# Kernel tuning notes

Measured on AMD Instinct MI355X. Metric: run time of the kernel, lower is better.

Reference implementation:

```python
import jax, jax.numpy as jnp
import numpy as np

D_MODEL = 1024
NUM_HEADS = 16
DEPTH = D_MODEL // NUM_HEADS


def setup_inputs() -> dict:
    key = jax.random.key(0)
    ks = jax.random.split(key, 9)
    B, S = 2, 2048
    s = 1.0 / np.sqrt(D_MODEL)
    return {
        "x": jax.random.normal(ks[0], (B, S, D_MODEL), dtype=jnp.float32),
        "wq": jax.random.normal(ks[1], (D_MODEL, D_MODEL), dtype=jnp.float32) * s,
        "bq": jnp.zeros((D_MODEL,), dtype=jnp.float32),
        "wk": jax.random.normal(ks[2], (D_MODEL, D_MODEL), dtype=jnp.float32) * s,
        "bk": jnp.zeros((D_MODEL,), dtype=jnp.float32),
        "wv": jax.random.normal(ks[3], (D_MODEL, D_MODEL), dtype=jnp.float32) * s,
        "bv": jnp.zeros((D_MODEL,), dtype=jnp.float32),
        "wo": jax.random.normal(ks[4], (D_MODEL, D_MODEL), dtype=jnp.float32) * s,
        "bo": jnp.zeros((D_MODEL,), dtype=jnp.float32),
    }


def _split_heads(t):
    # [B, S, D] -> [B, H, S, depth]
    B, S, _ = t.shape
    return t.reshape(B, S, NUM_HEADS, DEPTH).transpose(0, 2, 1, 3)


def reference(x, wq, bq, wk, bk, wv, bv, wo, bo):
    B, S, _ = x.shape
    q = _split_heads(x @ wq + bq)
    k = _split_heads(x @ wk + bk)
    v = _split_heads(x @ wv + bv)
    scale = 1.0 / jnp.sqrt(jnp.asarray(DEPTH, dtype=x.dtype))
    logits = jnp.einsum("bhsd,bhtd->bhst", q, k) * scale  # [B,H,S,S]
    attn = jax.nn.softmax(logits, axis=-1)
    ctx = jnp.einsum("bhst,bhtd->bhsd", attn, v)  # [B,H,S,depth]
    concat = ctx.transpose(0, 2, 1, 3).reshape(B, S, D_MODEL)
    return concat @ wo + bo
```

## Files before the change

### kernel.cpp

```cpp
#include <hip/hip_runtime.h>
#include <hip/hip_bf16.h>

typedef __bf16 bf16;
typedef __bf16 bf16x4 __attribute__((ext_vector_type(4)));
typedef __bf16 bf16x8 __attribute__((ext_vector_type(8)));
typedef float f32x4 __attribute__((ext_vector_type(4)));

typedef __attribute__((address_space(3))) void lds_void;
typedef const __attribute__((address_space(1))) void gbl_void;

#define D_MODEL 1024
#define NHEAD 16
#define DEPTH 64
#define SEQ 2048
#define BATCH 2
#define NTOK (BATCH * SEQ)

#define Q_SCALE 0.18033688f

__global__ __launch_bounds__(256) void prep(const float* __restrict__ w0,
                                            const float* __restrict__ w1,
                                            const float* __restrict__ w2,
                                            const float* __restrict__ w3,
                                            const float* __restrict__ x,
                                            bf16* __restrict__ wtb,
                                            bf16* __restrict__ xb) {
    int z = blockIdx.z;
    int tx = threadIdx.x, ty = threadIdx.y;
    if (z < 4) {
        const float* w = (z == 0) ? w0 : (z == 1) ? w1 : (z == 2) ? w2 : w3;
        bf16* d = wtb + (size_t)z * D_MODEL * D_MODEL;
        __shared__ float tile[32][33];
        int c0 = blockIdx.x * 32;
        int r0 = blockIdx.y * 32;
#pragma unroll
        for (int i = 0; i < 4; i++)
            tile[ty + i * 8][tx] = w[(size_t)(r0 + ty + i * 8) * D_MODEL + c0 + tx];
        __syncthreads();
#pragma unroll
        for (int i = 0; i < 4; i++)
            d[(size_t)(c0 + ty + i * 8) * D_MODEL + r0 + tx] = (bf16)tile[tx][ty + i * 8];
    } else {
        int t = ty * 32 + tx;
        size_t i = ((size_t)(z - 4) * 1024 + blockIdx.y * 32 + blockIdx.x) * 256 + t;
        float4 v = ((const float4*)x)[i];
        bf16x4 o = {(bf16)v.x, (bf16)v.y, (bf16)v.z, (bf16)v.w};
        *(bf16x4*)&xb[i * 4] = o;
    }
}

__global__ __launch_bounds__(512, 2) void qkv_gemm(const bf16* __restrict__ xb,
                                                   const bf16* __restrict__ wtb,
                                                   const float* __restrict__ bq,
                                                   const float* __restrict__ bk,
                                                   const float* __restrict__ bv,
                                                   bf16* __restrict__ q,
                                                   bf16* __restrict__ k,
                                                   bf16* __restrict__ v) {
    __shared__ bf16 sm[65536];

    const int flat = blockIdx.x;
    const int wg = (flat & 7) * 24 + (flat >> 3);
    const int mt = wg & 15, nt = wg >> 4;
    const int row0 = mt << 8;
    const int z = nt >> 2;
    const int nb = (nt & 3) << 8;

    const int tid = threadIdx.x;
    const int lane = tid & 63, wave = tid >> 6;
    const int wm = wave >> 2, wn = wave & 3;
    const int quad = lane >> 4, l16 = lane & 15;
    const int kch = ((quad ^ ((l16 >> 1) & 3)) << 3);

    const int srow = lane >> 2;
    const int scg = (lane & 3) ^ ((lane >> 3) & 3);
    const int stDst = wave * 1024 + lane * 8;

    const bf16* Ag = xb + (size_t)(row0 + wave * 32 + srow) * D_MODEL + scg * 8;
    const bf16* Bg = wtb + (size_t)z * D_MODEL * D_MODEL
                   + (size_t)(nb + wave * 32 + srow) * D_MODEL + scg * 8;

    f32x4 acc[8][4] = {};
    bf16x8 bfr[4];

#define GLL(SRC, DST) __builtin_amdgcn_global_load_lds((gbl_void*)(SRC), (lds_void*)(DST), 16, 0, 0)
#define STG_A(T_, KQ_, BUF_) { \
    const bf16* s_ = Ag + (T_) * 64 + (KQ_) * 32; \
    bf16* d_ = sm + (BUF_) * 16384 + (KQ_) * 8192 + stDst; \
    GLL(s_, d_); GLL(s_ + 16 * D_MODEL, d_ + 512); }
#define STG_B(T_, KQ_, BUF_) { \
    const bf16* s_ = Bg + (T_) * 64 + (KQ_) * 32; \
    bf16* d_ = sm + 32768 + (BUF_) * 16384 + (KQ_) * 8192 + stDst; \
    GLL(s_, d_); GLL(s_ + 16 * D_MODEL, d_ + 512); }
#define WAIT6 { asm volatile("s_waitcnt vmcnt(6)" ::: "memory"); }
#define NOW

#define PHASE(BUF_, KQ_, MQ_, STG_STMT, WAIT_STMT) { \
    bf16x8 af[4]; \
    const int ab_ = (BUF_) * 16384 + (KQ_) * 8192 + (wm * 128 + (MQ_) * 64 + l16) * 32 + kch; \
    _Pragma("unroll") \
    for (int i_ = 0; i_ < 4; i_++) af[i_] = *(const bf16x8*)&sm[ab_ + i_ * 512]; \
    if ((MQ_) == 0) { \
        const int bb_ = 32768 + (BUF_) * 16384 + (KQ_) * 8192 + (wn * 64 + l16) * 32 + kch; \
        _Pragma("unroll") \
        for (int j_ = 0; j_ < 4; j_++) bfr[j_] = *(const bf16x8*)&sm[bb_ + j_ * 512]; \
    } \
    STG_STMT; \
    WAIT_STMT; \
    __builtin_amdgcn_sched_barrier(0); \
    __builtin_amdgcn_s_barrier(); \
    __builtin_amdgcn_s_setprio(1); \
    _Pragma("unroll") \
    for (int i_ = 0; i_ < 4; i_++) \
        _Pragma("unroll") \
        for (int j_ = 0; j_ < 4; j_++) \
            acc[(MQ_) * 4 + i_][j_] = __builtin_amdgcn_mfma_f32_16x16x32_bf16( \
                af[i_], bfr[j_], acc[(MQ_) * 4 + i_][j_], 0, 0, 0); \
    __builtin_amdgcn_s_setprio(0); \
    __builtin_amdgcn_sched_barrier(0); \
    __builtin_amdgcn_s_barrier(); }

    STG_B(0, 0, 0);
    STG_A(0, 0, 0);
    STG_B(0, 1, 0);
    STG_A(0, 1, 0);
    asm volatile("s_waitcnt vmcnt(4)" ::: "memory");
    STG_B(1, 0, 1);
    STG_A(1, 0, 1);
    STG_B(1, 1, 1);
    asm volatile("s_waitcnt vmcnt(6)" ::: "memory");
    __builtin_amdgcn_sched_barrier(0);
    __builtin_amdgcn_s_barrier();

#pragma unroll 1
    for (int it = 0; it < 8; ++it) {
        const int t1 = 2 * it + 1;
        const int t2 = (2 * it + 2) & 15;
        const int t3 = (2 * it + 3) & 15;
        PHASE(0, 0, 0, STG_A(t1, 1, 1), NOW)
        PHASE(0, 0, 1, STG_B(t2, 0, 0), NOW)
        PHASE(0, 1, 0, STG_A(t2, 0, 0), NOW)
        PHASE(0, 1, 1, STG_B(t2, 1, 0), WAIT6)
        PHASE(1, 0, 0, STG_A(t2, 1, 0), NOW)
        PHASE(1, 0, 1, STG_B(t3, 0, 1), NOW)
        PHASE(1, 1, 0, STG_A(t3, 0, 1), NOW)
        PHASE(1, 1, 1, STG_B(t3, 1, 1), WAIT6)
    }

#undef PHASE
#undef WAIT6
#undef NOW
#undef STG_A
#undef STG_B
#undef GLL

    const float* bias = (z == 0) ? bq : (z == 1) ? bk : bv;
    const int bI = row0 >> 11;
    const int sBase = row0 & 2047;
    if (z < 2) {
        bf16* dst = (z == 0) ? q : k;
        const float scl = (z == 0) ? Q_SCALE : 1.0f;
#pragma unroll
        for (int j = 0; j < 4; j++) {
            const int f = nb + wn * 64 + j * 16 + l16;
            const float bi = bias[f];
            const int hh = f >> 6, d = f & 63;
            bf16* dcol = dst + ((size_t)(bI * NHEAD + hh) * SEQ) * DEPTH + d;
#pragma unroll
            for (int mi = 0; mi < 8; mi++) {
                const int s0 = sBase + wm * 128 + (mi >> 2) * 64 + (mi & 3) * 16 + quad * 4;
#pragma unroll
                for (int r = 0; r < 4; r++)
                    dcol[(size_t)(s0 + r) * DEPTH] = (bf16)((acc[mi][j][r] + bi) * scl);
            }
        }
    } else {
#pragma unroll
        for (int j = 0; j < 4; j++) {
            const int f = nb + wn * 64 + j * 16 + l16;
            const float bi = bias[f];
            const int hh = f >> 6, d = f & 63;
            bf16* vrow = v + ((size_t)(bI * NHEAD + hh) * DEPTH + d) * SEQ;
#pragma unroll
            for (int mi = 0; mi < 8; mi++) {
                const int s0 = sBase + wm * 128 + (mi >> 2) * 64 + (mi & 3) * 16 + quad * 4;
                f32x4 a = acc[mi][j];
                bf16x4 ob = {(bf16)(a[0] + bi), (bf16)(a[1] + bi),
                             (bf16)(a[2] + bi), (bf16)(a[3] + bi)};
                *(bf16x4*)&vrow[s0] = ob;
            }
        }
    }
}

__global__ __launch_bounds__(256) void attn(const bf16* __restrict__ q,
                                            const bf16* __restrict__ k,
                                            const bf16* __restrict__ v,
                                            bf16* __restrict__ ctx) {
    __shared__ __align__(16) bf16 smb[32768];
    const int tid = threadIdx.x;
    const int lane = tid & 63, wave = tid >> 6;
    const int quad = lane >> 4, l16 = lane & 15;
    const int bh = blockIdx.x;
    const int q0 = blockIdx.y * 64;
    const size_t hb = (size_t)bh * SEQ * DEPTH;
    const bf16* qh = q + hb;
    const bf16* kh = k + hb;
    const bf16* vh = v + hb;

    bf16x8 bq_[4][2];
#pragma unroll
    for (int n = 0; n < 4; n++) {
        int qrow = q0 + n * 16 + l16;
#pragma unroll
        for (int c = 0; c < 2; c++)
            bq_[n][c] = *(const bf16x8*)&qh[(size_t)qrow * DEPTH + c * 32 + quad * 8];
    }

    f32x4 ov[4][4] = {};
    f32x4 lv = {};

    const int wb = wave * 8192;
    const int kchS = (lane & 7) ^ (((lane >> 3) & 3) << 1);
    const int vchS = (lane & 3) ^ ((lane >> 2) & 3);
    const int krdL = ((l16 >> 2) << 3) + (l16 & 3);
    const int ksw = ((l16 & 3) << 1) | ((l16 >> 2) & 1);
    const int vsw = (quad ^ (l16 & 3)) << 3;

#define GLL(SRC, DST) __builtin_amdgcn_global_load_lds((gbl_void*)(SRC), (lds_void*)(DST), 16, 0, 0)

#define STAGE(BUF_, T_) { \
    _Pragma("unroll") \
    for (int o_ = 0; o_ < 4; o_++) { \
        const bf16* s_ = kh + (size_t)((T_) + wave * 32 + o_ * 8 + (lane >> 3)) * DEPTH \
                       + ((kchS ^ (o_ & 1)) << 3); \
        GLL(s_, smb + wb + (BUF_) * 2048 + o_ * 512 + lane * 8); \
    } \
    _Pragma("unroll") \
    for (int o_ = 0; o_ < 4; o_++) { \
        const bf16* s_ = vh + (size_t)(o_ * 16 + (lane >> 2)) * SEQ + (T_) + wave * 32 \
                       + (vchS << 3); \
        GLL(s_, smb + wb + 4096 + (BUF_) * 2048 + o_ * 512 + lane * 8); \
    } }

#define COMPUTE(BUF_) { \
    f32x4 s[2][4] = {}; \
    __builtin_amdgcn_s_setprio(1); \
    _Pragma("unroll") \
    for (int c_ = 0; c_ < 2; c_++) \
        _Pragma("unroll") \
        for (int h_ = 0; h_ < 2; h_++) { \
            bf16x8 kf = *(const bf16x8*)&smb[wb + (BUF_) * 2048 + (krdL + h_ * 4) * 64 \
                                             + ((((c_ << 2) | quad) ^ ksw) << 3)]; \
            _Pragma("unroll") \
            for (int n_ = 0; n_ < 4; n_++) \
                s[h_][n_] = __builtin_amdgcn_mfma_f32_16x16x32_bf16(kf, bq_[n_][c_], s[h_][n_], 0, 0, 0); \
        } \
    __builtin_amdgcn_s_setprio(0); \
    bf16x8 pb[4]; \
    _Pragma("unroll") \
    for (int n_ = 0; n_ < 4; n_++) { \
        float e0 = __builtin_amdgcn_exp2f(s[0][n_][0]); \
        float e1 = __builtin_amdgcn_exp2f(s[0][n_][1]); \
        float e2 = __builtin_amdgcn_exp2f(s[0][n_][2]); \
        float e3 = __builtin_amdgcn_exp2f(s[0][n_][3]); \
        float e4 = __builtin_amdgcn_exp2f(s[1][n_][0]); \
        float e5 = __builtin_amdgcn_exp2f(s[1][n_][1]); \
        float e6 = __builtin_amdgcn_exp2f(s[1][n_][2]); \
        float e7 = __builtin_amdgcn_exp2f(s[1][n_][3]); \
        pb[n_][0] = (bf16)e0; pb[n_][1] = (bf16)e1; \
        pb[n_][2] = (bf16)e2; pb[n_][3] = (bf16)e3; \
        pb[n_][4] = (bf16)e4; pb[n_][5] = (bf16)e5; \
        pb[n_][6] = (bf16)e6; pb[n_][7] = (bf16)e7; \
        lv[n_] += ((e0 + e1) + (e2 + e3)) + ((e4 + e5) + (e6 + e7)); \
    } \
    __builtin_amdgcn_s_setprio(1); \
    _Pragma("unroll") \
    for (int t_ = 0; t_ < 4; t_++) { \
        bf16x8 vf = *(const bf16x8*)&smb[wb + 4096 + (BUF_) * 2048 + (t_ * 16 + l16) * 32 + vsw]; \
        _Pragma("unroll") \
        for (int n_ = 0; n_ < 4; n_++) \
            ov[t_][n_] = __builtin_amdgcn_mfma_f32_16x16x32_bf16(vf, pb[n_], ov[t_][n_], 0, 0, 0); \
    } \
    __builtin_amdgcn_s_setprio(0); }

#define WAITV(N_) { asm volatile("s_waitcnt vmcnt(" #N_ ")" ::: "memory"); }
#define SB0 __builtin_amdgcn_sched_barrier(0)

    STAGE(0, 0);
#pragma unroll 1
    for (int tt = 0; tt < SEQ - 256; tt += 256) {
        STAGE(1, tt + 128);
        WAITV(8); SB0;
        COMPUTE(0); SB0;
        STAGE(0, tt + 256);
        WAITV(8); SB0;
        COMPUTE(1); SB0;
    }
    STAGE(1, SEQ - 128);
    WAITV(8); SB0;
    COMPUTE(0); SB0;
    WAITV(0); SB0;
    COMPUTE(1);

#undef SB0
#undef WAITV
#undef COMPUTE
#undef STAGE
#undef GLL

    f32x4* Red  = (f32x4*)smb;
    f32x4* Lred = (f32x4*)((char*)smb + 32768);
    __syncthreads();
#pragma unroll
    for (int tt = 0; tt < 8; tt++)
        Red[(tt * 4 + wave) * 64 + lane] = ov[tt >> 2][tt & 3];
    Lred[wave * 64 + lane] = lv;
    __syncthreads();
    f32x4 ls = {};
#pragma unroll
    for (int w_ = 0; w_ < 4; w_++)
#pragma unroll
        for (int qd = 0; qd < 4; qd++)
            ls += Lred[w_ * 64 + qd * 16 + l16];
    const int b = bh >> 4, hh = bh & 15;
    const int wb1 = wave & 1;
#pragma unroll
    for (int u = 0; u < 2; u++) {
        int tt = wave * 2 + u;
        f32x4 sv = Red[(tt * 4 + 0) * 64 + lane] + Red[(tt * 4 + 1) * 64 + lane]
                 + Red[(tt * 4 + 2) * 64 + lane] + Red[(tt * 4 + 3) * 64 + lane];
        int n = wb1 * 2 + u, t = wave >> 1;
        float iv = 1.0f / (wb1 ? ls[2 + u] : ls[u]);
        bf16x4 ob = {(bf16)(sv[0] * iv), (bf16)(sv[1] * iv),
                     (bf16)(sv[2] * iv), (bf16)(sv[3] * iv)};
        size_t off = ((size_t)(b * SEQ + q0 + n * 16 + l16)) * D_MODEL
                   + hh * 64 + t * 16 + quad * 4;
        *(bf16x4*)&ctx[off] = ob;
    }
    __syncthreads();
#pragma unroll
    for (int tt = 8; tt < 16; tt++)
        Red[((tt - 8) * 4 + wave) * 64 + lane] = ov[tt >> 2][tt & 3];
    __syncthreads();
#pragma unroll
    for (int u = 0; u < 2; u++) {
        int rt = wave * 2 + u;
        f32x4 sv = Red[(rt * 4 + 0) * 64 + lane] + Red[(rt * 4 + 1) * 64 + lane]
                 + Red[(rt * 4 + 2) * 64 + lane] + Red[(rt * 4 + 3) * 64 + lane];
        int n = wb1 * 2 + u, t = 2 + (wave >> 1);
        float iv = 1.0f / (wb1 ? ls[2 + u] : ls[u]);
        bf16x4 ob = {(bf16)(sv[0] * iv), (bf16)(sv[1] * iv),
                     (bf16)(sv[2] * iv), (bf16)(sv[3] * iv)};
        size_t off = ((size_t)(b * SEQ + q0 + n * 16 + l16)) * D_MODEL
                   + hh * 64 + t * 16 + quad * 4;
        *(bf16x4*)&ctx[off] = ob;
    }
}

__global__ __launch_bounds__(256) void out_gemm(const bf16* __restrict__ ctx,
                                                const bf16* __restrict__ wot,
                                                const float* __restrict__ bo,
                                                float* __restrict__ out) {
    __shared__ bf16 As[64 * 32];
    __shared__ bf16 Bs[128 * 32];
    const int tid = threadIdx.x;
    const int lane = tid & 63, wave = tid >> 6;
    const int quad = lane >> 4, l16 = lane & 15;
    const int srow = lane >> 2, selem = (lane & 3) * 8;
    int row0 = blockIdx.y * 64, col0 = blockIdx.x * 128;
    f32x4 acc[4][2] = {};

    for (int k0 = 0; k0 < D_MODEL; k0 += 32) {
        __syncthreads();
        {
            const bf16* ga = ctx + (size_t)(row0 + wave * 16 + srow) * D_MODEL + k0 + selem;
            __builtin_amdgcn_global_load_lds((gbl_void*)ga, (lds_void*)(As + wave * 512 + lane * 8), 16, 0, 0);
        }
#pragma unroll
        for (int t = 0; t < 2; t++) {
            int m = wave * 2 + t;
            const bf16* gb = wot + (size_t)(col0 + m * 16 + srow) * D_MODEL + k0 + selem;
            __builtin_amdgcn_global_load_lds((gbl_void*)gb, (lds_void*)(Bs + m * 512 + lane * 8), 16, 0, 0);
        }
        __syncthreads();
        bf16x8 af[4], bfr[2];
#pragma unroll
        for (int i = 0; i < 4; i++)
            af[i] = *(const bf16x8*)&As[(i * 16 + l16) * 32 + quad * 8];
#pragma unroll
        for (int j = 0; j < 2; j++)
            bfr[j] = *(const bf16x8*)&Bs[(wave * 32 + j * 16 + l16) * 32 + quad * 8];
#pragma unroll
        for (int i = 0; i < 4; i++)
#pragma unroll
            for (int j = 0; j < 2; j++)
                acc[i][j] = __builtin_amdgcn_mfma_f32_16x16x32_bf16(af[i], bfr[j], acc[i][j], 0, 0, 0);
    }
#pragma unroll
    for (int i = 0; i < 4; i++)
#pragma unroll
        for (int j = 0; j < 2; j++) {
            int colg = col0 + wave * 32 + j * 16 + l16;
            float bi = bo[colg];
            int rbase = row0 + i * 16 + quad * 4;
#pragma unroll
            for (int r = 0; r < 4; r++)
                out[(size_t)(rbase + r) * D_MODEL + colg] = acc[i][j][r] + bi;
        }
}

extern "C" void kernel_launch(void* const* d_in, const int* in_sizes, int n_in,
                              void* d_out, int out_size, void* d_ws, size_t ws_size,
                              hipStream_t stream) {
    const float* x  = (const float*)d_in[0];
    const float* wq = (const float*)d_in[1];
    const float* bq = (const float*)d_in[2];
    const float* wk = (const float*)d_in[3];
    const float* bk = (const float*)d_in[4];
    const float* wv = (const float*)d_in[5];
    const float* bv = (const float*)d_in[6];
    const float* wo = (const float*)d_in[7];
    const float* bo = (const float*)d_in[8];
    float* out = (float*)d_out;

    const size_t MB = 1024 * 1024;
    char* ws = (char*)d_ws;
    bf16* xb  = (bf16*)(ws);
    bf16* wtb = (bf16*)(ws + 8 * MB);
    bf16* qb  = (bf16*)(ws + 16 * MB);
    bf16* kb  = (bf16*)(ws + 24 * MB);
    bf16* vb  = (bf16*)(ws + 32 * MB);
    bf16* ctx = (bf16*)(ws + 40 * MB);

    prep<<<dim3(32, 32, 8), dim3(32, 8), 0, stream>>>(wq, wk, wv, wo, x, wtb, xb);
    qkv_gemm<<<dim3(192), dim3(512), 0, stream>>>(xb, wtb, bq, bk, bv, qb, kb, vb);
    attn<<<dim3(BATCH * NHEAD, SEQ / 64), 256, 0, stream>>>(qb, kb, vb, ctx);
    out_gemm<<<dim3(8, 64), 256, 0, stream>>>(ctx, wtb + 3 * (size_t)D_MODEL * D_MODEL, bo, out);
}
```

Measured before the change: 187.2 us.

## Stagger attention KV tile order per wave and double-buffer larger out-projection tiles

The attention loop now rotates the starting KV tile by wave index, so each wave walks the 16 key/value tiles in a different order under a unified double-buffered loop. The output GEMM moves from 64x128 tiles to 128x128 tiles with 4x4 MFMA accumulators per wave, double-buffered async global-to-LDS loads, an XOR swizzle on the LDS layout to avoid bank conflicts, and raised MFMA priority. This aims to raise data reuse and overlap loads with compute in the final projection, and to spread the attention loads over more distinct addresses. The trade-off is more registers and LDS per block and half as many blocks in the output GEMM.

```diff
diff --git a/kernel.cpp b/kernel.cpp
--- a/kernel.cpp
+++ b/kernel.cpp
@@ -287,21 +287,20 @@
 #define WAITV(N_) { asm volatile("s_waitcnt vmcnt(" #N_ ")" ::: "memory"); }
 #define SB0 __builtin_amdgcn_sched_barrier(0)
 
-    STAGE(0, 0);
+    const int tb = wave << 2;
+    STAGE(0, ((tb) & 15) * 128);
 #pragma unroll 1
-    for (int tt = 0; tt < SEQ - 256; tt += 256) {
-        STAGE(1, tt + 128);
-        WAITV(8); SB0;
-        COMPUTE(0); SB0;
-        STAGE(0, tt + 256);
-        WAITV(8); SB0;
-        COMPUTE(1); SB0;
-    }
-    STAGE(1, SEQ - 128);
-    WAITV(8); SB0;
-    COMPUTE(0); SB0;
-    WAITV(0); SB0;
-    COMPUTE(1);
+    for (int i = 0; i < 16; i++) {
+        if (i < 15) {
+            STAGE((i + 1) & 1, ((tb + i + 1) & 15) * 128);
+            WAITV(8);
+        } else {
+            WAITV(0);
+        }
+        SB0;
+        COMPUTE(i & 1);
+        SB0;
+    }
 
 #undef SB0
 #undef WAITV
@@ -362,48 +361,66 @@
                                                 const bf16* __restrict__ wot,
                                                 const float* __restrict__ bo,
                                                 float* __restrict__ out) {
-    __shared__ bf16 As[64 * 32];
-    __shared__ bf16 Bs[128 * 32];
+    __shared__ __align__(16) bf16 sm[2][2][4096];
     const int tid = threadIdx.x;
     const int lane = tid & 63, wave = tid >> 6;
     const int quad = lane >> 4, l16 = lane & 15;
-    const int srow = lane >> 2, selem = (lane & 3) * 8;
-    int row0 = blockIdx.y * 64, col0 = blockIdx.x * 128;
-    f32x4 acc[4][2] = {};
-
-    for (int k0 = 0; k0 < D_MODEL; k0 += 32) {
-        __syncthreads();
-        {
-            const bf16* ga = ctx + (size_t)(row0 + wave * 16 + srow) * D_MODEL + k0 + selem;
-            __builtin_amdgcn_global_load_lds((gbl_void*)ga, (lds_void*)(As + wave * 512 + lane * 8), 16, 0, 0);
+    const int wm = (wave & 1) << 6, wn = (wave >> 1) << 6;
+    const int kch = (quad ^ ((l16 >> 1) & 3)) << 3;
+    const int srow = tid >> 2;
+    const int scg = (tid & 3) ^ ((tid >> 3) & 3);
+    const int row0 = blockIdx.y * 128, col0 = blockIdx.x * 128;
+    f32x4 acc[4][4] = {};
+
+    const bf16* Ag = ctx + (size_t)(row0 + srow) * D_MODEL + scg * 8;
+    const bf16* Bg = wot + (size_t)(col0 + srow) * D_MODEL + scg * 8;
+
+#define GLL(SRC, DST) __builtin_amdgcn_global_load_lds((gbl_void*)(SRC), (lds_void*)(DST), 16, 0, 0)
+#define STG(BUF_, K_) { \
+    GLL(Ag + (K_), &sm[BUF_][0][0] + tid * 8); \
+    GLL(Ag + (K_) + 64 * D_MODEL, &sm[BUF_][0][0] + 2048 + tid * 8); \
+    GLL(Bg + (K_), &sm[BUF_][1][0] + tid * 8); \
+    GLL(Bg + (K_) + 64 * D_MODEL, &sm[BUF_][1][0] + 2048 + tid * 8); }
+
+    STG(0, 0);
+#pragma unroll 1
+    for (int kk = 0; kk < 32; kk++) {
+        if (kk < 31) {
+            STG((kk + 1) & 1, (kk + 1) * 32);
+            asm volatile("s_waitcnt vmcnt(4)" ::: "memory");
+        } else {
+            asm volatile("s_waitcnt vmcnt(0)" ::: "memory");
         }
-#pragma unroll
-        for (int t = 0; t < 2; t++) {
-            int m = wave * 2 + t;
-            const bf16* gb = wot + (size_t)(col0 + m * 16 + srow) * D_MODEL + k0 + selem;
-            __builtin_amdgcn_global_load_lds((gbl_void*)gb, (lds_void*)(Bs + m * 512 + lane * 8), 16, 0, 0);
-        }
-        __syncthreads();
-        bf16x8 af[4], bfr[2];
+        __builtin_amdgcn_sched_barrier(0);
+        __builtin_amdgcn_s_barrier();
+        bf16x8 af[4], bfr[4];
+        const int bs = kk & 1;
 #pragma unroll
         for (int i = 0; i < 4; i++)
-            af[i] = *(const bf16x8*)&As[(i * 16 + l16) * 32 + quad * 8];
-#pragma unroll
-        for (int j = 0; j < 2; j++)
-            bfr[j] = *(const bf16x8*)&Bs[(wave * 32 + j * 16 + l16) * 32 + quad * 8];
+            af[i] = *(const bf16x8*)&sm[bs][0][(wm + i * 16 + l16) * 32 + kch];
+#pragma unroll
+        for (int j = 0; j < 4; j++)
+            bfr[j] = *(const bf16x8*)&sm[bs][1][(wn + j * 16 + l16) * 32 + kch];
+        __builtin_amdgcn_s_setprio(1);
 #pragma unroll
         for (int i = 0; i < 4; i++)
 #pragma unroll
-            for (int j = 0; j < 2; j++)
+            for (int j = 0; j < 4; j++)
                 acc[i][j] = __builtin_amdgcn_mfma_f32_16x16x32_bf16(af[i], bfr[j], acc[i][j], 0, 0, 0);
-    }
+        __builtin_amdgcn_s_setprio(0);
+        __builtin_amdgcn_sched_barrier(0);
+        __builtin_amdgcn_s_barrier();
+    }
+#undef STG
+#undef GLL
+
 #pragma unroll
     for (int i = 0; i < 4; i++)
 #pragma unroll
-        for (int j = 0; j < 2; j++) {
-            int colg = col0 + wave * 32 + j * 16 + l16;
+        for (int j = 0; j < 4; j++) {
+            int colg = col0 + wn + j * 16 + l16;
             float bi = bo[colg];
-            int rbase = row0 + i * 16 + quad * 4;
+            int rbase = row0 + wm + i * 16 + quad * 4;
 #pragma unroll
             for (int r = 0; r < 4; r++)
                 out[(size_t)(rbase + r) * D_MODEL + colg] = acc[i][j][r] + bi;
@@ -436,5 +453,5 @@
     prep<<<dim3(32, 32, 8), dim3(32, 8), 0, stream>>>(wq, wk, wv, wo, x, wtb, xb);
     qkv_gemm<<<dim3(192), dim3(512), 0, stream>>>(xb, wtb, bq, bk, bv, qb, kb, vb);
     attn<<<dim3(BATCH * NHEAD, SEQ / 64), 256, 0, stream>>>(qb, kb, vb, ctx);
-    out_gemm<<<dim3(8, 64), 256, 0, stream>>>(ctx, wtb + 3 * (size_t)D_MODEL * D_MODEL, bo, out);
+    out_gemm<<<dim3(8, 32), 256, 0, stream>>>(ctx, wtb + 3 * (size_t)D_MODEL * D_MODEL, bo, out);
 }
```

Result: no change. 190.5 us (+1.7%).
